# Kernel optimization log

Hardware: AMD Instinct MI355X
Metric: run time of the kernel (lower is better)

The kernel has to match this reference:

```python
import jax, jax.numpy as jnp
import numpy as np

B, N, D_IN, D_OUT = 8, 2048, 256, 256
BN_EPS = 1e-5
SELU_ALPHA = 1.6732632423543772
SELU_SCALE = 1.0507009873554805


def setup_inputs() -> dict:
    key = jax.random.key(0)
    k1, k2, k3, k4 = jax.random.split(key, 4)
    lim_lin = 1.0 / np.sqrt(D_IN)
    return {
        "x": jax.random.normal(k1, (B, N, D_IN), dtype=jnp.float32),
        "w_map": jax.random.uniform(k2, (D_IN,), jnp.float32, -lim_lin, lim_lin),
        "w_att": jax.random.uniform(k3, (D_OUT, D_IN), jnp.float32, -lim_lin, lim_lin),
        "w_res": jax.random.uniform(k4, (D_OUT, D_IN), jnp.float32, -lim_lin, lim_lin),
        "gamma": jnp.ones((D_OUT,), jnp.float32),
        "beta": jnp.zeros((D_OUT,), jnp.float32),
    }


def _selu(x):
    x_clamped = jnp.clip(x, -10.0, 10.0)
    return SELU_SCALE * jnp.where(x > 0, x, SELU_ALPHA * (jnp.exp(x_clamped) - 1.0))


def reference(x, w_map, w_att, w_res, gamma, beta):
    # scores[b,i,j] = sum_d w_map[d] * x[b,i,d] * x[b,j,d]  (== W_map(x_i*x_j))
    scores = jnp.einsum("bid,bjd->bij", x * w_map, x)  # [B,N,N]
    attn = jax.nn.softmax(scores, axis=-1)
    aggregated = jnp.einsum("bij,bjd->bid", attn, x)  # [B,N,D]
    out = aggregated @ w_att.T + x @ w_res.T  # [B,N,D_OUT]
    # BatchNorm1d in training mode: stats over (batch, nodes) per channel, biased var
    mean = jnp.mean(out, axis=(0, 1))
    var = jnp.mean(jnp.square(out - mean), axis=(0, 1))
    out = (out - mean) * jax.lax.rsqrt(var + BN_EPS) * gamma + beta
    return _selu(out)
```

## Files before the change

kernel.cpp:

```cpp
#include <hip/hip_runtime.h>
#include <hip/hip_bf16.h>


typedef __attribute__((ext_vector_type(8))) short  bf16x8;
typedef __attribute__((ext_vector_type(4))) float  f32x4;

#define MFMA16(a, b, c) __builtin_amdgcn_mfma_f32_16x16x32_bf16((a), (b), (c), 0, 0, 0)

constexpr int   NB = 8, NN = 2048, ND = 256;
constexpr int   ROWS = NB * NN;
constexpr float BN_EPS = 1e-5f;
constexpr float SELU_ALPHA = 1.6732632423543772f;
constexpr float SELU_SCALE = 1.0507009873554805f;

__device__ __forceinline__ unsigned short f2bf(float f) {
  union { float f; unsigned int u; } v; v.f = f;
  unsigned int u = v.u;
  u += 0x7FFFu + ((u >> 16) & 1u);
  return (unsigned short)(u >> 16);
}
__device__ __forceinline__ float bf2f(unsigned short h) {
  union { float f; unsigned int u; } v; v.u = ((unsigned int)h) << 16;
  return v.f;
}

__device__ __forceinline__ void async_copy16(const unsigned short* g, unsigned short* l) {
  __builtin_amdgcn_global_load_lds(
      (const __attribute__((address_space(1))) void*)g,
      (__attribute__((address_space(3))) void*)l, 16, 0, 0);
}

__global__ __launch_bounds__(256) void k0_prep(const float* __restrict__ x,
                                               unsigned short* __restrict__ AX,
                                               unsigned short* __restrict__ Xt) {
  __shared__ unsigned short Ls[64 * 264];
  const int t = threadIdx.x;
  const int b = blockIdx.x & 7, rt = blockIdx.x >> 3;
  const int grb = b * NN + rt * 64;
  const int c = (t & 31) * 8, r0 = t >> 5;
#pragma unroll
  for (int q = 0; q < 8; ++q) {
    int r = r0 + q * 8;
    const float* xp = x + (size_t)(grb + r) * 256 + c;
    float4 a = *(const float4*)xp;
    float4 d = *(const float4*)(xp + 4);
    union { unsigned short s[8]; uint4 v; } xb;
    xb.s[0] = f2bf(a.x); xb.s[1] = f2bf(a.y); xb.s[2] = f2bf(a.z); xb.s[3] = f2bf(a.w);
    xb.s[4] = f2bf(d.x); xb.s[5] = f2bf(d.y); xb.s[6] = f2bf(d.z); xb.s[7] = f2bf(d.w);
    *(uint4*)(AX + (size_t)(grb + r) * 512 + 256 + c) = xb.v;
    *(uint4*)&Ls[r * 264 + c] = xb.v;
  }
  __syncthreads();
  unsigned short* dst = Xt + ((size_t)b * 256 + t) * 2048 + rt * 64;
#pragma unroll
  for (int k = 0; k < 8; ++k) {
    union { unsigned short s[8]; uint4 v; } o;
#pragma unroll
    for (int j = 0; j < 8; ++j) o.s[j] = Ls[(k * 8 + j) * 264 + t];
    *(uint4*)(dst + k * 8) = o.v;
  }
}

__global__ __launch_bounds__(256) void k0_wc(const float* __restrict__ w_att,
                                             const float* __restrict__ w_res,
                                             unsigned short* __restrict__ WC,
                                             float* __restrict__ sums) {
  if (blockIdx.x == 0 && threadIdx.x < 128)
    ((float4*)sums)[threadIdx.x] = make_float4(0.f, 0.f, 0.f, 0.f);
  int f = (blockIdx.x * 256 + threadIdx.x) * 8;
  int c = f >> 9, k = f & 511;
  const float* src = (k < 256) ? (w_att + c * 256 + k) : (w_res + c * 256 + (k - 256));
  float4 a = *(const float4*)src;
  float4 b = *(const float4*)(src + 4);
  union { unsigned short s[8]; uint4 v; } o;
  o.s[0] = f2bf(a.x); o.s[1] = f2bf(a.y); o.s[2] = f2bf(a.z); o.s[3] = f2bf(a.w);
  o.s[4] = f2bf(b.x); o.s[5] = f2bf(b.y); o.s[6] = f2bf(b.z); o.s[7] = f2bf(b.w);
  *(uint4*)(WC + f) = o.v;
}

__global__ __launch_bounds__(512, 2) void k1_attn(const float* __restrict__ w_map,
                                                  const unsigned short* AX,
                                                  const unsigned short* __restrict__ Xt,
                                                  unsigned short* AXw) {
  __shared__ unsigned short Ks[2][2][32 * 256];
  __shared__ unsigned short Vt[2][2][256 * 32];
  __shared__ unsigned short Psw[8][16 * 40];

  const int t = threadIdx.x;
  const int w = t >> 6, lane = t & 63, l15 = lane & 15, quad = lane >> 4;
  const int g = w >> 2, wg = w & 3;
  const int b = blockIdx.x & 7, it = blockIdx.x >> 3;
  const int gib = b * NN + it * 64;
  const unsigned short* Xtb = Xt + (size_t)b * 256 * 2048;
  const unsigned short* AXr = AX + (size_t)b * NN * 512 + 256;
  const int jgbase = g * 1024;

  int ksOff[4], vtOff[4];
#pragma unroll
  for (int q = 0; q < 4; ++q) {
    int j = wg * 8 + q * 2 + (lane >> 5);
    int ck = (lane & 31) ^ (j & 7);
    ksOff[q] = j * 512 + ck * 8;
    int d = wg * 64 + q * 16 + (lane >> 2);
    int cv = (lane & 3) ^ ((d >> 1) & 3);
    vtOff[q] = d * 2048 + cv * 8;
  }
  const int ldsOff = wg * 2048 + lane * 8;

  bf16x8 qf[8];
  {
    const unsigned short* xrow = AXr + (size_t)(it * 64 + wg * 16 + l15) * 512;
#pragma unroll
    for (int kc = 0; kc < 8; ++kc) {
      bf16x8 xb = *(const bf16x8*)(xrow + kc * 32 + quad * 8);
      const float* wp = w_map + kc * 32 + quad * 8;
      float4 w0 = *(const float4*)wp, w1 = *(const float4*)(wp + 4);
      float wv[8] = {w0.x, w0.y, w0.z, w0.w, w1.x, w1.y, w1.z, w1.w};
      bf16x8 q;
#pragma unroll
      for (int i = 0; i < 8; ++i)
        q[i] = (short)f2bf(bf2f((unsigned short)xb[i]) * wv[i]);
      qf[kc] = q;
    }
  }

  const f32x4 fz = {0.f, 0.f, 0.f, 0.f};
  f32x4 oacc[16];
#pragma unroll
  for (int i = 0; i < 16; ++i) oacc[i] = fz;
  f32x4 oL = fz;

  bf16x8 onesFrag;
  {
    short o1 = (l15 == 0) ? (short)0x3F80 : (short)0;
#pragma unroll
    for (int i = 0; i < 8; ++i) onesFrag[i] = o1;
  }

#pragma unroll
  for (int q = 0; q < 4; ++q)
    async_copy16(AXr + (size_t)jgbase * 512 + ksOff[q], &Ks[g][0][ldsOff + q * 512]);
#pragma unroll
  for (int q = 0; q < 4; ++q)
    async_copy16(Xtb + jgbase + vtOff[q], &Vt[g][0][ldsOff + q * 512]);

  for (int jt = 0; jt < 32; ++jt) {
    const int cur = jt & 1;
    __syncthreads();
    if (jt < 31) {
      const int jb1 = jgbase + (jt + 1) * 32;
#pragma unroll
      for (int q = 0; q < 4; ++q)
        async_copy16(AXr + (size_t)jb1 * 512 + ksOff[q], &Ks[g][cur ^ 1][ldsOff + q * 512]);
#pragma unroll
      for (int q = 0; q < 4; ++q)
        async_copy16(Xtb + jb1 + vtOff[q], &Vt[g][cur ^ 1][ldsOff + q * 512]);
    }
#pragma unroll
    for (int jm = 0; jm < 2; ++jm) {
      const int j = jm * 16 + l15;
      f32x4 s = fz;
#pragma unroll
      for (int kc = 0; kc < 8; ++kc) {
        int ckk = kc * 4 + quad;
        bf16x8 kf = *(const bf16x8*)&Ks[g][cur][j * 256 + ((ckk ^ (j & 7)) * 8)];
        s = MFMA16(kf, qf[kc], s);
      }
      ushort4 pk;
      pk.x = f2bf(__expf(s[0])); pk.y = f2bf(__expf(s[1]));
      pk.z = f2bf(__expf(s[2])); pk.w = f2bf(__expf(s[3]));
      *(ushort4*)&Psw[w][l15 * 40 + jm * 16 + quad * 4] = pk;
    }
    bf16x8 af = *(const bf16x8*)&Psw[w][l15 * 40 + quad * 8];
#pragma unroll
    for (int nti = 0; nti < 16; ++nti) {
      const int d = nti * 16 + l15;
      bf16x8 vf = *(const bf16x8*)&Vt[g][cur][d * 32 + ((quad ^ ((d >> 1) & 3)) * 8)];
      oacc[nti] = MFMA16(af, vf, oacc[nti]);
    }
    oL = MFMA16(af, onesFrag, oL);
  }

  __syncthreads();
  float* Obuf = (float*)&Ks[0][0][0];
  float* Lb   = (float*)&Vt[0][0][0];
  if (g == 1) {
#pragma unroll
    for (int nti = 0; nti < 16; ++nti)
#pragma unroll
      for (int r = 0; r < 4; ++r) {
        int row = quad * 4 + r;
        Obuf[wg * 4096 + row * 256 + (((nti + quad) & 15) << 4) + l15] = oacc[nti][r];
      }
    if (l15 == 0) {
#pragma unroll
      for (int r = 0; r < 4; ++r) Lb[wg * 16 + quad * 4 + r] = oL[r];
    }
  }
  __syncthreads();
  if (g == 0) {
    float ls[4];
#pragma unroll
    for (int r = 0; r < 4; ++r) ls[r] = Lb[wg * 16 + quad * 4 + r];
#pragma unroll
    for (int nti = 0; nti < 16; ++nti)
#pragma unroll
      for (int r = 0; r < 4; ++r) {
        int row = quad * 4 + r;
        oacc[nti][r] += Obuf[wg * 4096 + row * 256 + (((nti + quad) & 15) << 4) + l15];
      }
    float li[4];
#pragma unroll
    for (int r = 0; r < 4; ++r)
      li[r] = 1.0f / (__shfl(oL[r], lane & 48) + ls[r]);
#pragma unroll
    for (int nti = 0; nti < 16; ++nti) {
      const int gcol = nti * 16 + l15;
#pragma unroll
      for (int r = 0; r < 4; ++r) {
        const int grow = gib + wg * 16 + quad * 4 + r;
        AXw[(size_t)grow * 512 + gcol] = f2bf(oacc[nti][r] * li[r]);
      }
    }
  }
}

__global__ __launch_bounds__(256, 2) void k2_gemm(const unsigned short* __restrict__ AX,
                                                  const unsigned short* __restrict__ WC,
                                                  float* __restrict__ out,
                                                  float* __restrict__ sums) {
  __shared__ unsigned short As[128 * 72];
  __shared__ unsigned short Bs[64 * 72];
  __shared__ float cs[64], cq[64];
  const int t = threadIdx.x;
  const int w = t >> 6, lane = t & 63, l15 = lane & 15, quad = lane >> 4;
  const int m0 = (blockIdx.x >> 2) * 128, n0 = (blockIdx.x & 3) * 64;
  if (t < 64) { cs[t] = 0.f; cq[t] = 0.f; }

  const f32x4 fz = {0.f, 0.f, 0.f, 0.f};
  f32x4 acc[4][2];
#pragma unroll
  for (int i = 0; i < 4; ++i) { acc[i][0] = fz; acc[i][1] = fz; }

  for (int kk = 0; kk < 512; kk += 64) {
    __syncthreads();
#pragma unroll
    for (int q = 0; q < 4; ++q) {
      int idx = t + q * 256;
      int row = idx >> 3, koff = (idx & 7) * 8;
      *(uint4*)&As[row * 72 + koff] = *(const uint4*)(AX + (size_t)(m0 + row) * 512 + kk + koff);
    }
#pragma unroll
    for (int q = 0; q < 2; ++q) {
      int idx = t + q * 256;
      int row = idx >> 3, koff = (idx & 7) * 8;
      *(uint4*)&Bs[row * 72 + koff] = *(const uint4*)(WC + (size_t)(n0 + row) * 512 + kk + koff);
    }
    __syncthreads();
#pragma unroll
    for (int kc = 0; kc < 2; ++kc) {
      bf16x8 b0 = *(const bf16x8*)&Bs[((w >> 1) * 32 + l15) * 72 + kc * 32 + quad * 8];
      bf16x8 b1 = *(const bf16x8*)&Bs[((w >> 1) * 32 + 16 + l15) * 72 + kc * 32 + quad * 8];
#pragma unroll
      for (int mt = 0; mt < 4; ++mt) {
        bf16x8 af = *(const bf16x8*)&As[((w & 1) * 64 + mt * 16 + l15) * 72 + kc * 32 + quad * 8];
        acc[mt][0] = MFMA16(af, b0, acc[mt][0]);
        acc[mt][1] = MFMA16(af, b1, acc[mt][1]);
      }
    }
  }
#pragma unroll
  for (int mt = 0; mt < 4; ++mt)
#pragma unroll
    for (int nt = 0; nt < 2; ++nt)
#pragma unroll
      for (int r = 0; r < 4; ++r) {
        int grow = m0 + (w & 1) * 64 + mt * 16 + quad * 4 + r;
        int gcol = n0 + (w >> 1) * 32 + nt * 16 + l15;
        out[(size_t)grow * 256 + gcol] = acc[mt][nt][r];
      }
#pragma unroll
  for (int nt = 0; nt < 2; ++nt) {
    float a = 0.f, b2 = 0.f;
#pragma unroll
    for (int mt = 0; mt < 4; ++mt)
#pragma unroll
      for (int r = 0; r < 4; ++r) {
        float v = acc[mt][nt][r];
        a += v; b2 += v * v;
      }
    a += __shfl_xor(a, 16);  a += __shfl_xor(a, 32);
    b2 += __shfl_xor(b2, 16); b2 += __shfl_xor(b2, 32);
    if (quad == 0) {
      int ci = (w >> 1) * 32 + nt * 16 + l15;
      atomicAdd(&cs[ci], a);
      atomicAdd(&cq[ci], b2);
    }
  }
  __syncthreads();
  if (t < 64) {
    atomicAdd(&sums[n0 + t], cs[t]);
    atomicAdd(&sums[256 + n0 + t], cq[t]);
  }
}

__global__ __launch_bounds__(256) void k4_bn_selu(float* __restrict__ out,
                                                  const float* __restrict__ sums,
                                                  const float* __restrict__ gamma,
                                                  const float* __restrict__ beta) {
  int f = (blockIdx.x * 256 + threadIdx.x) * 8;
  int c = f & 255;
  const float inv_m = 1.0f / 16384.0f;
  float4 v0 = *(const float4*)(out + f);
  float4 v1 = *(const float4*)(out + f + 4);
  float vv[8] = {v0.x, v0.y, v0.z, v0.w, v1.x, v1.y, v1.z, v1.w};
#pragma unroll
  for (int k = 0; k < 8; ++k) {
    int ch = c + k;
    float mean = sums[ch] * inv_m;
    float var = sums[256 + ch] * inv_m - mean * mean;
    float y = (vv[k] - mean) * rsqrtf(var + BN_EPS) * gamma[ch] + beta[ch];
    float yc = fminf(fmaxf(y, -10.f), 10.f);
    float r = (y > 0.f) ? y : (SELU_ALPHA * (expf(yc) - 1.0f));
    vv[k] = SELU_SCALE * r;
  }
  float4 o0 = {vv[0], vv[1], vv[2], vv[3]};
  float4 o1 = {vv[4], vv[5], vv[6], vv[7]};
  *(float4*)(out + f) = o0;
  *(float4*)(out + f + 4) = o1;
}

extern "C" void kernel_launch(void* const* d_in, const int* in_sizes, int n_in,
                              void* d_out, int out_size, void* d_ws, size_t ws_size,
                              hipStream_t stream) {
  const float* x     = (const float*)d_in[0];
  const float* w_map = (const float*)d_in[1];
  const float* w_att = (const float*)d_in[2];
  const float* w_res = (const float*)d_in[3];
  const float* gamma = (const float*)d_in[4];
  const float* beta  = (const float*)d_in[5];
  float* out = (float*)d_out;

  unsigned short* AX = (unsigned short*)d_ws;
  unsigned short* Xt = AX + (size_t)ROWS * 512;
  unsigned short* WC = Xt + (size_t)NB * 256 * 2048;
  float* sums = (float*)(WC + 256 * 512);

  k0_prep<<<256, 256, 0, stream>>>(x, AX, Xt);
  k0_wc<<<64, 256, 0, stream>>>(w_att, w_res, WC, sums);
  k1_attn<<<256, 512, 0, stream>>>(w_map, AX, Xt, AX);
  k2_gemm<<<512, 256, 0, stream>>>(AX, WC, out, sums);
  k4_bn_selu<<<2048, 256, 0, stream>>>(out, sums, gamma, beta);
}
```

Measured before the change: 163.0 us.

## Merge weight prep into prep kernel, double-buffer GEMM, precompute BN scale

Folds the weight-conversion and sums-zeroing kernel into the activation prep kernel as extra blocks, which removes one launch. The output GEMM now double-buffers its tiles using async global-to-LDS copies with an XOR-swizzled layout, so loads overlap the MFMA work and the padding used to avoid bank conflicts is no longer needed. The BN+SELU kernel computes a per-channel scale and shift once per block in shared memory instead of recomputing mean, variance and rsqrt for every element. The GEMM and BN kernels are small next to the attention kernel, so the overall effect is limited.

```diff
diff --git a/kernel.cpp b/kernel.cpp
--- a/kernel.cpp
+++ b/kernel.cpp
@@ -31,10 +31,29 @@
 }
 
 __global__ __launch_bounds__(256) void k0_prep(const float* __restrict__ x,
+                                               const float* __restrict__ w_att,
+                                               const float* __restrict__ w_res,
                                                unsigned short* __restrict__ AX,
-                                               unsigned short* __restrict__ Xt) {
+                                               unsigned short* __restrict__ Xt,
+                                               unsigned short* __restrict__ WC,
+                                               float* __restrict__ sums) {
   __shared__ unsigned short Ls[64 * 264];
   const int t = threadIdx.x;
+  if (blockIdx.x >= 256) {
+    const int bid = blockIdx.x - 256;
+    if (bid == 0 && t < 128)
+      ((float4*)sums)[t] = make_float4(0.f, 0.f, 0.f, 0.f);
+    int f = (bid * 256 + t) * 8;
+    int c = f >> 9, k = f & 511;
+    const float* src = (k < 256) ? (w_att + c * 256 + k) : (w_res + c * 256 + (k - 256));
+    float4 a = *(const float4*)src;
+    float4 b = *(const float4*)(src + 4);
+    union { unsigned short s[8]; uint4 v; } o;
+    o.s[0] = f2bf(a.x); o.s[1] = f2bf(a.y); o.s[2] = f2bf(a.z); o.s[3] = f2bf(a.w);
+    o.s[4] = f2bf(b.x); o.s[5] = f2bf(b.y); o.s[6] = f2bf(b.z); o.s[7] = f2bf(b.w);
+    *(uint4*)(WC + f) = o.v;
+    return;
+  }
   const int b = blockIdx.x & 7, rt = blockIdx.x >> 3;
   const int grb = b * NN + rt * 64;
   const int c = (t & 31) * 8, r0 = t >> 5;
@@ -61,23 +80,6 @@
   }
 }
 
-__global__ __launch_bounds__(256) void k0_wc(const float* __restrict__ w_att,
-                                             const float* __restrict__ w_res,
-                                             unsigned short* __restrict__ WC,
-                                             float* __restrict__ sums) {
-  if (blockIdx.x == 0 && threadIdx.x < 128)
-    ((float4*)sums)[threadIdx.x] = make_float4(0.f, 0.f, 0.f, 0.f);
-  int f = (blockIdx.x * 256 + threadIdx.x) * 8;
-  int c = f >> 9, k = f & 511;
-  const float* src = (k < 256) ? (w_att + c * 256 + k) : (w_res + c * 256 + (k - 256));
-  float4 a = *(const float4*)src;
-  float4 b = *(const float4*)(src + 4);
-  union { unsigned short s[8]; uint4 v; } o;
-  o.s[0] = f2bf(a.x); o.s[1] = f2bf(a.y); o.s[2] = f2bf(a.z); o.s[3] = f2bf(a.w);
-  o.s[4] = f2bf(b.x); o.s[5] = f2bf(b.y); o.s[6] = f2bf(b.z); o.s[7] = f2bf(b.w);
-  *(uint4*)(WC + f) = o.v;
-}
-
 __global__ __launch_bounds__(512, 2) void k1_attn(const float* __restrict__ w_map,
                                                   const unsigned short* AX,
                                                   const unsigned short* __restrict__ Xt,
@@ -229,41 +231,62 @@
                                                   const unsigned short* __restrict__ WC,
                                                   float* __restrict__ out,
                                                   float* __restrict__ sums) {
-  __shared__ unsigned short As[128 * 72];
-  __shared__ unsigned short Bs[64 * 72];
+  __shared__ unsigned short As[2][128 * 64];
+  __shared__ unsigned short Bs[2][64 * 64];
   __shared__ float cs[64], cq[64];
   const int t = threadIdx.x;
   const int w = t >> 6, lane = t & 63, l15 = lane & 15, quad = lane >> 4;
   const int m0 = (blockIdx.x >> 2) * 128, n0 = (blockIdx.x & 3) * 64;
   if (t < 64) { cs[t] = 0.f; cq[t] = 0.f; }
 
+  int aOff[4], bOff[2];
+#pragma unroll
+  for (int q = 0; q < 4; ++q) {
+    int u = t + q * 256, row = u >> 3, c = (u & 7) ^ (row & 7);
+    aOff[q] = (m0 + row) * 512 + c * 8;
+  }
+#pragma unroll
+  for (int q = 0; q < 2; ++q) {
+    int u = t + q * 256, row = u >> 3, c = (u & 7) ^ (row & 7);
+    bOff[q] = (n0 + row) * 512 + c * 8;
+  }
+  const int ldsA = t * 8;
+  const int ldsB = t * 8;
+
   const f32x4 fz = {0.f, 0.f, 0.f, 0.f};
   f32x4 acc[4][2];
 #pragma unroll
   for (int i = 0; i < 4; ++i) { acc[i][0] = fz; acc[i][1] = fz; }
 
-  for (int kk = 0; kk < 512; kk += 64) {
+#pragma unroll
+  for (int q = 0; q < 4; ++q)
+    async_copy16(AX + (size_t)aOff[q], &As[0][ldsA + q * 2048]);
+#pragma unroll
+  for (int q = 0; q < 2; ++q)
+    async_copy16(WC + (size_t)bOff[q], &Bs[0][ldsB + q * 2048]);
+
+  for (int ki = 0; ki < 8; ++ki) {
+    const int cur = ki & 1;
     __syncthreads();
-#pragma unroll
-    for (int q = 0; q < 4; ++q) {
-      int idx = t + q * 256;
-      int row = idx >> 3, koff = (idx & 7) * 8;
-      *(uint4*)&As[row * 72 + koff] = *(const uint4*)(AX + (size_t)(m0 + row) * 512 + kk + koff);
-    }
-#pragma unroll
-    for (int q = 0; q < 2; ++q) {
-      int idx = t + q * 256;
-      int row = idx >> 3, koff = (idx & 7) * 8;
-      *(uint4*)&Bs[row * 72 + koff] = *(const uint4*)(WC + (size_t)(n0 + row) * 512 + kk + koff);
-    }
-    __syncthreads();
+    if (ki < 7) {
+      const int kk = (ki + 1) * 64;
+#pragma unroll
+      for (int q = 0; q < 4; ++q)
+        async_copy16(AX + (size_t)(aOff[q] + kk), &As[cur ^ 1][ldsA + q * 2048]);
+#pragma unroll
+      for (int q = 0; q < 2; ++q)
+        async_copy16(WC + (size_t)(bOff[q] + kk), &Bs[cur ^ 1][ldsB + q * 2048]);
+    }
 #pragma unroll
     for (int kc = 0; kc < 2; ++kc) {
-      bf16x8 b0 = *(const bf16x8*)&Bs[((w >> 1) * 32 + l15) * 72 + kc * 32 + quad * 8];
-      bf16x8 b1 = *(const bf16x8*)&Bs[((w >> 1) * 32 + 16 + l15) * 72 + kc * 32 + quad * 8];
+      const int c = kc * 4 + quad;
+      const int rb0 = (w >> 1) * 32 + l15, rb1 = rb0 + 16;
+      bf16x8 b0 = *(const bf16x8*)&Bs[cur][rb0 * 64 + ((c ^ (rb0 & 7)) * 8)];
+      bf16x8 b1 = *(const bf16x8*)&Bs[cur][rb1 * 64 + ((c ^ (rb1 & 7)) * 8)];
 #pragma unroll
       for (int mt = 0; mt < 4; ++mt) {
-        bf16x8 af = *(const bf16x8*)&As[((w & 1) * 64 + mt * 16 + l15) * 72 + kc * 32 + quad * 8];
+        const int ra = (w & 1) * 64 + mt * 16 + l15;
+        bf16x8 af = *(const bf16x8*)&As[cur][ra * 64 + ((c ^ (ra & 7)) * 8)];
         acc[mt][0] = MFMA16(af, b0, acc[mt][0]);
         acc[mt][1] = MFMA16(af, b1, acc[mt][1]);
       }
@@ -308,18 +331,26 @@
                                                   const float* __restrict__ sums,
                                                   const float* __restrict__ gamma,
                                                   const float* __restrict__ beta) {
-  int f = (blockIdx.x * 256 + threadIdx.x) * 8;
+  __shared__ float sc[256], sh[256];
+  const int t = threadIdx.x;
+  {
+    const float inv_m = 1.0f / 16384.0f;
+    float mean = sums[t] * inv_m;
+    float var = sums[256 + t] * inv_m - mean * mean;
+    float s = rsqrtf(var + BN_EPS) * gamma[t];
+    sc[t] = s;
+    sh[t] = beta[t] - mean * s;
+  }
+  __syncthreads();
+  int f = (blockIdx.x * 256 + t) * 8;
   int c = f & 255;
-  const float inv_m = 1.0f / 16384.0f;
   float4 v0 = *(const float4*)(out + f);
   float4 v1 = *(const float4*)(out + f + 4);
   float vv[8] = {v0.x, v0.y, v0.z, v0.w, v1.x, v1.y, v1.z, v1.w};
 #pragma unroll
   for (int k = 0; k < 8; ++k) {
     int ch = c + k;
-    float mean = sums[ch] * inv_m;
-    float var = sums[256 + ch] * inv_m - mean * mean;
-    float y = (vv[k] - mean) * rsqrtf(var + BN_EPS) * gamma[ch] + beta[ch];
+    float y = vv[k] * sc[ch] + sh[ch];
     float yc = fminf(fmaxf(y, -10.f), 10.f);
     float r = (y > 0.f) ? y : (SELU_ALPHA * (expf(yc) - 1.0f));
     vv[k] = SELU_SCALE * r;
@@ -346,8 +377,7 @@
   unsigned short* WC = Xt + (size_t)NB * 256 * 2048;
   float* sums = (float*)(WC + 256 * 512);
 
-  k0_prep<<<256, 256, 0, stream>>>(x, AX, Xt);
-  k0_wc<<<64, 256, 0, stream>>>(w_att, w_res, WC, sums);
+  k0_prep<<<320, 256, 0, stream>>>(x, w_att, w_res, AX, Xt, WC, sums);
   k1_attn<<<256, 512, 0, stream>>>(w_map, AX, Xt, AX);
   k2_gemm<<<512, 256, 0, stream>>>(AX, WC, out, sums);
   k4_bn_selu<<<2048, 256, 0, stream>>>(out, sums, gamma, beta);
```

Result: no change. 163.0 us (+0.0%).
